# Optimization experiments

Measured on AMD Instinct MI355X. Metric: run time of the kernel, lower is better.

Reference implementation:

```python
import jax, jax.numpy as jnp
import numpy as np

B, L, D = 4, 4096, 1024
N_HEADS = 16
HEAD_SIZE = D // N_HEADS  # 64


def setup_inputs() -> dict:
    key = jax.random.key(0)
    k_x, k_w, k_m = jax.random.split(key, 3)
    x = jax.random.normal(k_x, (B, L, D), dtype=jnp.float32)
    # nn.Linear(D, 3*head_size, bias=False): weight (3*hs, D); store transposed (D, 3*hs)
    W_qkv = jax.random.normal(k_w, (D, 3 * HEAD_SIZE), dtype=jnp.float32) * (D ** -0.5)
    attn_mask = jax.random.randint(k_m, (B, L), 0, 2).astype(jnp.bool_)
    return {"x": x, "attn_mask": attn_mask, "W_qkv": W_qkv}


def reference(x, attn_mask, W_qkv):
    # x: (B, L, D); W_qkv: (D, 3*hs); attn_mask: (B, L) True = attend
    qkv = x @ W_qkv                                # (B, L, 3*hs)
    q, k, v = jnp.split(qkv, 3, axis=-1)           # each (B, L, hs)
    scale = HEAD_SIZE ** -0.5
    scores = jnp.einsum('bqd,bkd->bqk', q, k) * scale   # (B, L, L)
    neg_inf = jnp.finfo(scores.dtype).min
    scores = jnp.where(attn_mask[:, None, :], scores, neg_inf)
    weights = jax.nn.softmax(scores, axis=-1)      # (B, L, L)
    out = jnp.einsum('bqk,bkd->bqd', weights, v)   # (B, L, hs)
    return out
```

## Files before the change

### kernel.cpp

```cpp
#include <hip/hip_runtime.h>

typedef __bf16 bf16_t;
typedef __bf16 bf16x8 __attribute__((ext_vector_type(8)));
typedef __bf16 bf16x4 __attribute__((ext_vector_type(4)));
typedef float  f32x4  __attribute__((ext_vector_type(4)));
struct uint4_t { unsigned x, y, z, w; };

#define B_  4
#define L_  4096
#define D_  1024
#define HS  64
#define NQ  192
#define SCL2E 0.1803368801111204f
#define MFMA16 __builtin_amdgcn_mfma_f32_16x16x32_bf16

__global__ void detect_kernel(const unsigned char* mask, const unsigned short* xw,
                              int* flags) {
    __shared__ int c1, c23, cbad;
    int tid = threadIdx.x;
    if (tid == 0) { c1 = 0; c23 = 0; cbad = 0; }
    __syncthreads();
    uint4_t m[4];
#pragma unroll
    for (int i = 0; i < 4; ++i)
        m[i] = *(const uint4_t*)(mask + tid * 16 + i * 4096);
    int a = 0, bc = 0;
#pragma unroll
    for (int i = 0; i < 4; ++i) {
        const unsigned* w = (const unsigned*)&m[i];
#pragma unroll
        for (int j = 0; j < 4; ++j) {
            if (w[j] & 0x0000ff00u) a++;
            if (w[j] & 0xffff0000u) bc++;
        }
    }
    uint4_t xm = *(const uint4_t*)(xw + tid * 8);
    int bad = 0;
    const unsigned* xwv = (const unsigned*)&xm;
#pragma unroll
    for (int j = 0; j < 4; ++j)
#pragma unroll
        for (int h = 0; h < 2; ++h) {
            unsigned s = (xwv[j] >> (16 * h)) & 0xFFFFu;
            unsigned e = (s >> 7) & 0xFF;
            if (e > 150 || (e < 90 && e != 0)) bad++;
        }
    if (a)   atomicAdd(&c1, a);
    if (bc)  atomicAdd(&c23, bc);
    if (bad) atomicAdd(&cbad, bad);
    __syncthreads();
    if (tid == 0) {
        flags[0] = (c1 > 0) ? 1 : ((c23 > 0) ? 2 : 0);
        flags[1] = (cbad >= 64) ? 1 : 0;
    }
}

__global__ __launch_bounds__(256) void pack_w_kernel(const void* __restrict__ Win,
                                                     const int* __restrict__ flags,
                                                     bf16_t* __restrict__ Wtp) {
    int idx = blockIdx.x * 256 + threadIdx.x;
    if (idx >= 24576) return;
    int lane = idx & 63;
    int t    = (idx >> 6) & 3;
    int kc   = (idx >> 8) & 31;
    int ct   = idx >> 13;
    int n  = ct * 64 + t * 16 + (lane & 15);
    int k0 = kc * 32 + (lane >> 4) * 8;
    int f32 = flags[1];
    bf16x8 v;
#pragma unroll
    for (int j = 0; j < 8; ++j) {
        if (f32) v[j] = (bf16_t)(((const float*)Win)[(k0 + j) * NQ + n]);
        else     v[j] = ((const bf16_t*)Win)[(k0 + j) * NQ + n];
    }
    *(bf16x8*)(Wtp + (size_t)idx * 8) = v;
}

__global__ __launch_bounds__(256, 2) void qkv_gemm_kernel(const void* __restrict__ xin,
                                                          const int* __restrict__ flags,
                                                          const bf16_t* __restrict__ Wtp,
                                                          bf16_t* __restrict__ Qb,
                                                          bf16_t* __restrict__ Kb,
                                                          bf16_t* __restrict__ Vt) {
    __shared__ __align__(16) bf16_t xt[2][32 * 72];
    __shared__ __align__(16) bf16_t sqk[32 * 136];
    __shared__ __align__(16) bf16_t sv[64 * 40];

    int tid = threadIdx.x;
    int wave = tid >> 6, lane = tid & 63, quad = lane >> 4, l16 = lane & 15;
    int rg = wave & 1, ch = wave >> 1;
    int m0 = blockIdx.x * 32;
    int xf = flags[1];

    f32x4 acc[6] = {};
    bf16x8 xr, Ba[6], Bb[6];
    int srow = tid >> 3, soff = (tid & 7) * 8;

    auto stage_load = [&](int ks) {
        if (xf) {
            const float* xp = (const float*)xin + (size_t)(m0 + srow) * D_ + ks * 64 + soff;
            f32x4 lo = *(const f32x4*)xp, hi = *(const f32x4*)(xp + 4);
            xr[0] = (bf16_t)lo[0]; xr[1] = (bf16_t)lo[1];
            xr[2] = (bf16_t)lo[2]; xr[3] = (bf16_t)lo[3];
            xr[4] = (bf16_t)hi[0]; xr[5] = (bf16_t)hi[1];
            xr[6] = (bf16_t)hi[2]; xr[7] = (bf16_t)hi[3];
        } else {
            xr = *(const bf16x8*)((const bf16_t*)xin + (size_t)(m0 + srow) * D_ + ks * 64 + soff);
        }
    };
    auto stage_store = [&](int buf) {
        *(bf16x8*)&xt[buf][srow * 72 + soff] = xr;
    };
    auto loadB6 = [&](int k32, bf16x8* Bv) {
#pragma unroll
        for (int i = 0; i < 6; ++i) {
            int st = ch * 6 + i, ct2 = st >> 2, tt = st & 3;
            Bv[i] = *(const bf16x8*)(Wtp + ((size_t)(ct2 * 32 + k32) * 4 + tt) * 512 + lane * 8);
        }
    };
    auto compute6 = [&](int buf, int c, const bf16x8* Bv) {
        bf16x8 A = *(const bf16x8*)&xt[buf][(rg * 16 + l16) * 72 + c * 32 + quad * 8];
#pragma unroll
        for (int i = 0; i < 6; ++i)
            acc[i] = MFMA16(A, Bv[i], acc[i], 0, 0, 0);
    };

    stage_load(0); stage_store(0);
    loadB6(0, Ba);
    __syncthreads();
    for (int ks = 0; ks < 16; ++ks) {
        bool more = (ks + 1 < 16);
        if (more) stage_load(ks + 1);
        loadB6(2 * ks + 1, Bb);
        compute6(ks & 1, 0, Ba);
        if (more) loadB6(2 * ks + 2, Ba);
        compute6(ks & 1, 1, Bb);
        if (more) stage_store((ks + 1) & 1);
        __syncthreads();
    }

    int rowb = rg * 16 + quad * 4;
#pragma unroll
    for (int i = 0; i < 6; ++i) {
        int col = ch * 96 + i * 16 + l16;
#pragma unroll
        for (int r = 0; r < 4; ++r) {
            bf16_t hv = (bf16_t)acc[i][r];
            if (col < 128) sqk[(rowb + r) * 136 + col] = hv;
            else           sv[(col - 128) * 40 + rowb + r] = hv;
        }
    }
    __syncthreads();

    int bb = m0 >> 12, l0 = m0 & 4095;
#pragma unroll
    for (int it = 0; it < 2; ++it) {
        int c = tid + it * 256;
        int row = c >> 4, off = (c & 15) * 8;
        bf16x8 v = *(const bf16x8*)&sqk[row * 136 + off];
        if (off < 64) *(bf16x8*)(Qb + (size_t)(bb * L_ + l0 + row) * HS + off) = v;
        else          *(bf16x8*)(Kb + (size_t)(bb * L_ + l0 + row) * HS + off - 64) = v;
    }
    {
        int d = tid >> 2, off = (tid & 3) * 8;
        bf16x8 v = *(const bf16x8*)&sv[d * 40 + off];
        *(bf16x8*)(Vt + (size_t)(bb * HS + d) * L_ + l0 + off) = v;
    }
}

template<int NSPLIT>
__global__ __launch_bounds__(256, 4) void attn_kernel(const bf16_t* __restrict__ Qb,
                                                      const bf16_t* __restrict__ Kb,
                                                      const bf16_t* __restrict__ Vt,
                                                      const void* __restrict__ maskp,
                                                      const int* __restrict__ flags,
                                                      float* __restrict__ Opart,
                                                      float* __restrict__ lpart,
                                                      void* __restrict__ outv) {
    constexpr int KCH = L_ / NSPLIT;
    constexpr int NIT = KCH / 64;
    __shared__ __align__(16) bf16_t ktile[2][64 * 72];
    __shared__ __align__(16) bf16_t plds[4][32 * 72];
    __shared__ float mb[KCH];

    int tid = threadIdx.x, wave = tid >> 6, lane = tid & 63;
    int quad = lane >> 4, l16 = lane & 15;
    int grp = blockIdx.x % (B_ * NSPLIT);
    int qt  = blockIdx.x / (B_ * NSPLIT);
    int s = grp / B_, b = grp % B_;
    int q0 = qt * 128;
    int kbase = s * KCH;

    const float NEGINF = -__builtin_inff();
    int mkind = flags[0];
    if (mkind == 1) {
        const unsigned char* mp = (const unsigned char*)maskp + b * L_ + kbase;
        for (int i = tid; i < KCH; i += 256) mb[i] = mp[i] ? 0.0f : NEGINF;
    } else if (mkind == 2) {
        const float* mp = (const float*)maskp + b * L_ + kbase;
        for (int i = tid; i < KCH; i += 256) mb[i] = (mp[i] != 0.0f) ? 0.0f : NEGINF;
    } else {
        const int* mp = (const int*)maskp + b * L_ + kbase;
        for (int i = tid; i < KCH; i += 256) mb[i] = mp[i] ? 0.0f : NEGINF;
    }

    bf16x8 aQ[2][2];
#pragma unroll
    for (int rg = 0; rg < 2; ++rg) {
        const bf16_t* qp = Qb + (size_t)(b * L_ + q0 + wave * 32 + rg * 16 + l16) * HS + quad * 8;
        aQ[rg][0] = *(const bf16x8*)qp;
        aQ[rg][1] = *(const bf16x8*)(qp + 32);
    }

    const bf16_t* Kbase = Kb + (size_t)b * L_ * HS;
    const bf16_t* Vbase = Vt + (size_t)b * HS * L_;

    f32x4 O[2][4] = {};
    float lr[2][4] = {};
    bf16_t* pw = &plds[wave][0];
    bf16x8 kr[2];
    int srow = 0, soff = 0;

    auto kstage_load = [&](int t) {
#pragma unroll
        for (int j = 0; j < 2; ++j) {
            int c = tid + j * 256;
            int row = c >> 3, off = (c & 7) * 8;
            kr[j] = *(const bf16x8*)(Kbase + (size_t)(kbase + t * 64 + row) * HS + off);
        }
    };
    auto kstage_store = [&](int buf) {
#pragma unroll
        for (int j = 0; j < 2; ++j) {
            int c = tid + j * 256;
            int row = c >> 3, off = (c & 7) * 8;
            *(bf16x8*)&ktile[buf][row * 72 + off] = kr[j];
        }
    };
    (void)srow; (void)soff;

    kstage_load(0);
    kstage_store(0);
    __syncthreads();

    for (int t = 0; t < NIT; ++t) {
        int kb = kbase + t * 64;
        bool more = (t + 1 < NIT);
        if (more) kstage_load(t + 1);

        bf16x8 V0[4];
#pragma unroll
        for (int nt = 0; nt < 4; ++nt)
            V0[nt] = *(const bf16x8*)(Vbase + (size_t)(nt * 16 + l16) * L_ + kb + quad * 8);

        const bf16_t* kl = &ktile[t & 1][0];
#pragma unroll
        for (int h = 0; h < 2; ++h) {
            f32x4 sc[2][2];
#pragma unroll
            for (int s2 = 0; s2 < 2; ++s2) {
                int st = h * 2 + s2;
                bf16x8 kb0 = *(const bf16x8*)&kl[(st * 16 + l16) * 72 + quad * 8];
                bf16x8 kb1 = *(const bf16x8*)&kl[(st * 16 + l16) * 72 + 32 + quad * 8];
#pragma unroll
                for (int rg = 0; rg < 2; ++rg) {
                    f32x4 t0 = {};
                    t0 = MFMA16(aQ[rg][0], kb0, t0, 0, 0, 0);
                    t0 = MFMA16(aQ[rg][1], kb1, t0, 0, 0, 0);
                    sc[rg][s2] = t0;
                }
            }
#pragma unroll
            for (int s2 = 0; s2 < 2; ++s2) {
                int st = h * 2 + s2;
                float bl = mb[t * 64 + st * 16 + l16];
#pragma unroll
                for (int rg = 0; rg < 2; ++rg)
#pragma unroll
                    for (int r = 0; r < 4; ++r) {
                        float p = exp2f(fmaf(sc[rg][s2][r], SCL2E, bl));
                        lr[rg][r] += p;
                        pw[(rg * 16 + quad * 4 + r) * 72 + st * 16 + l16] = (bf16_t)p;
                    }
            }
        }

#pragma unroll
        for (int rg = 0; rg < 2; ++rg) {
            bf16x8 aP = *(const bf16x8*)&pw[(rg * 16 + l16) * 72 + quad * 8];
#pragma unroll
            for (int nt = 0; nt < 4; ++nt)
                O[rg][nt] = MFMA16(aP, V0[nt], O[rg][nt], 0, 0, 0);
        }
        bf16x8 V1[4];
#pragma unroll
        for (int nt = 0; nt < 4; ++nt)
            V1[nt] = *(const bf16x8*)(Vbase + (size_t)(nt * 16 + l16) * L_ + kb + 32 + quad * 8);
#pragma unroll
        for (int rg = 0; rg < 2; ++rg) {
            bf16x8 aP = *(const bf16x8*)&pw[(rg * 16 + l16) * 72 + 32 + quad * 8];
#pragma unroll
            for (int nt = 0; nt < 4; ++nt)
                O[rg][nt] = MFMA16(aP, V1[nt], O[rg][nt], 0, 0, 0);
        }

        if (more) kstage_store((t + 1) & 1);
        __syncthreads();
    }

    int of32 = flags[1];
#pragma unroll
    for (int rg = 0; rg < 2; ++rg)
#pragma unroll
        for (int r = 0; r < 4; ++r) {
            float sm = lr[rg][r];
            sm += __shfl_xor(sm, 1);
            sm += __shfl_xor(sm, 2);
            sm += __shfl_xor(sm, 4);
            sm += __shfl_xor(sm, 8);
            int row = q0 + wave * 32 + rg * 16 + quad * 4 + r;
            if (NSPLIT == 1) {
                float inv = 1.0f / sm;
                size_t base = (size_t)(b * L_ + row) * HS;
                if (of32) {
                    float* op = (float*)outv + base;
#pragma unroll
                    for (int nt = 0; nt < 4; ++nt) op[nt * 16 + l16] = O[rg][nt][r] * inv;
                } else {
                    bf16_t* op = (bf16_t*)outv + base;
#pragma unroll
                    for (int nt = 0; nt < 4; ++nt) op[nt * 16 + l16] = (bf16_t)(O[rg][nt][r] * inv);
                }
            } else {
                float* op = Opart + (size_t)s * (B_ * L_ * HS) + (size_t)(b * L_ + row) * HS;
#pragma unroll
                for (int nt = 0; nt < 4; ++nt) op[nt * 16 + l16] = O[rg][nt][r];
                if (l16 == 0) lpart[(size_t)s * (B_ * L_) + b * L_ + row] = sm;
            }
        }
}

__global__ __launch_bounds__(256) void reduce_kernel(const float* __restrict__ Opart,
                                                     const float* __restrict__ lpart,
                                                     const int* __restrict__ flags,
                                                     void* __restrict__ outv,
                                                     int nsplit) {
    int i4 = (blockIdx.x * 256 + threadIdx.x) * 4;
    int row = i4 >> 6;
    f32x4 acc = {};
    float lsum = 0.f;
    for (int s = 0; s < nsplit; ++s) {
        acc  += *(const f32x4*)&Opart[(size_t)s * (B_ * L_ * HS) + i4];
        lsum += lpart[(size_t)s * (B_ * L_) + row];
    }
    float inv = 1.0f / lsum;
    if (flags[1]) {
        f32x4 r = { acc[0] * inv, acc[1] * inv, acc[2] * inv, acc[3] * inv };
        *(f32x4*)&((float*)outv)[i4] = r;
    } else {
        bf16x4 r;
#pragma unroll
        for (int j = 0; j < 4; ++j) r[j] = (bf16_t)(acc[j] * inv);
        *(bf16x4*)&((bf16_t*)outv)[i4] = r;
    }
}

extern "C" void kernel_launch(void* const* d_in, const int* in_sizes, int n_in,
                              void* d_out, int out_size, void* d_ws, size_t ws_size,
                              hipStream_t stream) {
    (void)in_sizes; (void)n_in; (void)out_size;
    const void* x    = d_in[0];
    const void* mask = d_in[1];
    const void* W    = d_in[2];

    char* ws = (char*)d_ws;
    bf16_t* Qb    = (bf16_t*)(ws);
    bf16_t* Kb    = (bf16_t*)(ws + (2u << 20));
    bf16_t* Vt    = (bf16_t*)(ws + (4u << 20));
    bf16_t* Wtp   = (bf16_t*)(ws + (6u << 20));
    int*    flags = (int*)   (ws + (6u << 20) + (512u << 10));
    float*  Opart = (float*) (ws + (7u << 20));

    auto need = [](int ns) -> size_t {
        return (7u << 20) + (size_t)ns * (B_ * L_ * HS * 4)
                          + (size_t)ns * (B_ * L_ * 4) + 4096;
    };
    int nsplit = (ws_size >= need(8)) ? 8 : (ws_size >= need(4)) ? 4 : 1;
    float* lpart = (float*)(ws + (7u << 20) + (size_t)nsplit * (B_ * L_ * HS * 4));

    detect_kernel<<<1, 256, 0, stream>>>((const unsigned char*)mask,
                                         (const unsigned short*)x, flags);
    pack_w_kernel<<<96, 256, 0, stream>>>(W, flags, Wtp);
    qkv_gemm_kernel<<<512, 256, 0, stream>>>(x, flags, Wtp, Qb, Kb, Vt);
    if (nsplit == 8) {
        attn_kernel<8><<<32 * B_ * 8, 256, 0, stream>>>(Qb, Kb, Vt, mask, flags,
                                                        Opart, lpart, d_out);
        reduce_kernel<<<(B_ * L_ * HS) / 1024, 256, 0, stream>>>(Opart, lpart, flags,
                                                                 d_out, 8);
    } else if (nsplit == 4) {
        attn_kernel<4><<<32 * B_ * 4, 256, 0, stream>>>(Qb, Kb, Vt, mask, flags,
                                                        Opart, lpart, d_out);
        reduce_kernel<<<(B_ * L_ * HS) / 1024, 256, 0, stream>>>(Opart, lpart, flags,
                                                                 d_out, 4);
    } else {
        attn_kernel<1><<<32 * B_, 256, 0, stream>>>(Qb, Kb, Vt, mask, flags,
                                                    Opart, lpart, d_out);
    }
}
```

Before: 182.6 us.

## Fuse detect into weight pack, stage x in halves, compute softmax sum via MFMA

```diff
diff --git a/kernel.cpp b/kernel.cpp
--- a/kernel.cpp
+++ b/kernel.cpp
@@ -14,8 +14,11 @@
 #define SCL2E 0.1803368801111204f
 #define MFMA16 __builtin_amdgcn_mfma_f32_16x16x32_bf16
 
-__global__ void detect_kernel(const unsigned char* mask, const unsigned short* xw,
-                              int* flags) {
+__global__ __launch_bounds__(256) void pack_w_kernel(const void* __restrict__ Win,
+                                                     const unsigned char* __restrict__ mask,
+                                                     const unsigned short* __restrict__ xw,
+                                                     bf16_t* __restrict__ Wtp,
+                                                     int* __restrict__ flags) {
     __shared__ int c1, c23, cbad;
     int tid = threadIdx.x;
     if (tid == 0) { c1 = 0; c23 = 0; cbad = 0; }
@@ -49,24 +52,19 @@
     if (bc)  atomicAdd(&c23, bc);
     if (bad) atomicAdd(&cbad, bad);
     __syncthreads();
-    if (tid == 0) {
+    int f32 = (cbad >= 64) ? 1 : 0;
+    if (blockIdx.x == 0 && tid == 0) {
         flags[0] = (c1 > 0) ? 1 : ((c23 > 0) ? 2 : 0);
-        flags[1] = (cbad >= 64) ? 1 : 0;
-    }
-}
-
-__global__ __launch_bounds__(256) void pack_w_kernel(const void* __restrict__ Win,
-                                                     const int* __restrict__ flags,
-                                                     bf16_t* __restrict__ Wtp) {
-    int idx = blockIdx.x * 256 + threadIdx.x;
-    if (idx >= 24576) return;
+        flags[1] = f32;
+    }
+
+    int idx = blockIdx.x * 256 + tid;
     int lane = idx & 63;
     int t    = (idx >> 6) & 3;
     int kc   = (idx >> 8) & 31;
     int ct   = idx >> 13;
     int n  = ct * 64 + t * 16 + (lane & 15);
     int k0 = kc * 32 + (lane >> 4) * 8;
-    int f32 = flags[1];
     bf16x8 v;
 #pragma unroll
     for (int j = 0; j < 8; ++j) {
@@ -82,7 +80,7 @@
                                                           bf16_t* __restrict__ Qb,
                                                           bf16_t* __restrict__ Kb,
                                                           bf16_t* __restrict__ Vt) {
-    __shared__ __align__(16) bf16_t xt[2][32 * 72];
+    __shared__ __align__(16) bf16_t xs[32 * 520];
     __shared__ __align__(16) bf16_t sqk[32 * 136];
     __shared__ __align__(16) bf16_t sv[64 * 40];
 
@@ -93,50 +91,64 @@
     int xf = flags[1];
 
     f32x4 acc[6] = {};
-    bf16x8 xr, Ba[6], Bb[6];
-    int srow = tid >> 3, soff = (tid & 7) * 8;
-
-    auto stage_load = [&](int ks) {
-        if (xf) {
-            const float* xp = (const float*)xin + (size_t)(m0 + srow) * D_ + ks * 64 + soff;
-            f32x4 lo = *(const f32x4*)xp, hi = *(const f32x4*)(xp + 4);
-            xr[0] = (bf16_t)lo[0]; xr[1] = (bf16_t)lo[1];
-            xr[2] = (bf16_t)lo[2]; xr[3] = (bf16_t)lo[3];
-            xr[4] = (bf16_t)hi[0]; xr[5] = (bf16_t)hi[1];
-            xr[6] = (bf16_t)hi[2]; xr[7] = (bf16_t)hi[3];
-        } else {
-            xr = *(const bf16x8*)((const bf16_t*)xin + (size_t)(m0 + srow) * D_ + ks * 64 + soff);
-        }
-    };
-    auto stage_store = [&](int buf) {
-        *(bf16x8*)&xt[buf][srow * 72 + soff] = xr;
-    };
-    auto loadB6 = [&](int k32, bf16x8* Bv) {
+    bf16x8 Ba[6], Bb[6];
+
+    auto stage = [&](int h) {
+        bf16x8 tmp[8];
+#pragma unroll
+        for (int j = 0; j < 8; ++j) {
+            int c = tid + j * 256;
+            int row = c >> 6, off = (c & 63) * 8;
+            if (xf) {
+                const float* xp = (const float*)xin + (size_t)(m0 + row) * D_ + h * 512 + off;
+                f32x4 lo = *(const f32x4*)xp, hi = *(const f32x4*)(xp + 4);
+                tmp[j][0] = (bf16_t)lo[0]; tmp[j][1] = (bf16_t)lo[1];
+                tmp[j][2] = (bf16_t)lo[2]; tmp[j][3] = (bf16_t)lo[3];
+                tmp[j][4] = (bf16_t)hi[0]; tmp[j][5] = (bf16_t)hi[1];
+                tmp[j][6] = (bf16_t)hi[2]; tmp[j][7] = (bf16_t)hi[3];
+            } else {
+                tmp[j] = *(const bf16x8*)((const bf16_t*)xin + (size_t)(m0 + row) * D_ + h * 512 + off);
+            }
+        }
+#pragma unroll
+        for (int j = 0; j < 8; ++j) {
+            int c = tid + j * 256;
+            int row = c >> 6, off = (c & 63) * 8;
+            *(bf16x8*)&xs[row * 520 + off] = tmp[j];
+        }
+    };
+    auto loadB6 = [&](int ks, bf16x8* Bv) {
 #pragma unroll
         for (int i = 0; i < 6; ++i) {
             int st = ch * 6 + i, ct2 = st >> 2, tt = st & 3;
-            Bv[i] = *(const bf16x8*)(Wtp + ((size_t)(ct2 * 32 + k32) * 4 + tt) * 512 + lane * 8);
-        }
-    };
-    auto compute6 = [&](int buf, int c, const bf16x8* Bv) {
-        bf16x8 A = *(const bf16x8*)&xt[buf][(rg * 16 + l16) * 72 + c * 32 + quad * 8];
+            Bv[i] = *(const bf16x8*)(Wtp + ((size_t)(ct2 * 32 + ks) * 4 + tt) * 512 + lane * 8);
+        }
+    };
+    auto compute6 = [&](int ks, const bf16x8* Bv) {
+        bf16x8 A = *(const bf16x8*)&xs[(rg * 16 + l16) * 520 + (ks & 15) * 32 + quad * 8];
 #pragma unroll
         for (int i = 0; i < 6; ++i)
             acc[i] = MFMA16(A, Bv[i], acc[i], 0, 0, 0);
     };
 
-    stage_load(0); stage_store(0);
+    stage(0);
     loadB6(0, Ba);
     __syncthreads();
-    for (int ks = 0; ks < 16; ++ks) {
-        bool more = (ks + 1 < 16);
-        if (more) stage_load(ks + 1);
-        loadB6(2 * ks + 1, Bb);
-        compute6(ks & 1, 0, Ba);
-        if (more) loadB6(2 * ks + 2, Ba);
-        compute6(ks & 1, 1, Bb);
-        if (more) stage_store((ks + 1) & 1);
-        __syncthreads();
+#pragma unroll
+    for (int half = 0; half < 2; ++half) {
+        int base = half * 16;
+        for (int m = 0; m < 16; m += 2) {
+            int ks = base + m;
+            loadB6(ks + 1, Bb);
+            compute6(ks, Ba);
+            loadB6(ks + 2 <= 31 ? ks + 2 : 31, Ba);
+            compute6(ks + 1, Bb);
+        }
+        if (half == 0) {
+            __syncthreads();
+            stage(1);
+            __syncthreads();
+        }
     }
 
     int rowb = rg * 16 + quad * 4;
@@ -211,15 +223,17 @@
         aQ[rg][0] = *(const bf16x8*)qp;
         aQ[rg][1] = *(const bf16x8*)(qp + 32);
     }
+    bf16x8 ones;
+#pragma unroll
+    for (int j = 0; j < 8; ++j) ones[j] = (bf16_t)1.0f;
 
     const bf16_t* Kbase = Kb + (size_t)b * L_ * HS;
     const bf16_t* Vbase = Vt + (size_t)b * HS * L_;
 
     f32x4 O[2][4] = {};
-    float lr[2][4] = {};
+    f32x4 O5[2] = {};
     bf16_t* pw = &plds[wave][0];
     bf16x8 kr[2];
-    int srow = 0, soff = 0;
 
     auto kstage_load = [&](int t) {
 #pragma unroll
@@ -237,7 +251,6 @@
             *(bf16x8*)&ktile[buf][row * 72 + off] = kr[j];
         }
     };
-    (void)srow; (void)soff;
 
     kstage_load(0);
     kstage_store(0);
@@ -279,7 +292,6 @@
 #pragma unroll
                     for (int r = 0; r < 4; ++r) {
                         float p = exp2f(fmaf(sc[rg][s2][r], SCL2E, bl));
-                        lr[rg][r] += p;
                         pw[(rg * 16 + quad * 4 + r) * 72 + st * 16 + l16] = (bf16_t)p;
                     }
             }
@@ -291,6 +303,7 @@
 #pragma unroll
             for (int nt = 0; nt < 4; ++nt)
                 O[rg][nt] = MFMA16(aP, V0[nt], O[rg][nt], 0, 0, 0);
+            O5[rg] = MFMA16(aP, ones, O5[rg], 0, 0, 0);
         }
         bf16x8 V1[4];
 #pragma unroll
@@ -302,6 +315,7 @@
 #pragma unroll
             for (int nt = 0; nt < 4; ++nt)
                 O[rg][nt] = MFMA16(aP, V1[nt], O[rg][nt], 0, 0, 0);
+            O5[rg] = MFMA16(aP, ones, O5[rg], 0, 0, 0);
         }
 
         if (more) kstage_store((t + 1) & 1);
@@ -313,11 +327,7 @@
     for (int rg = 0; rg < 2; ++rg)
 #pragma unroll
         for (int r = 0; r < 4; ++r) {
-            float sm = lr[rg][r];
-            sm += __shfl_xor(sm, 1);
-            sm += __shfl_xor(sm, 2);
-            sm += __shfl_xor(sm, 4);
-            sm += __shfl_xor(sm, 8);
+            float sm = O5[rg][r];
             int row = q0 + wave * 32 + rg * 16 + quad * 4 + r;
             if (NSPLIT == 1) {
                 float inv = 1.0f / sm;
@@ -388,9 +398,8 @@
     int nsplit = (ws_size >= need(8)) ? 8 : (ws_size >= need(4)) ? 4 : 1;
     float* lpart = (float*)(ws + (7u << 20) + (size_t)nsplit * (B_ * L_ * HS * 4));
 
-    detect_kernel<<<1, 256, 0, stream>>>((const unsigned char*)mask,
-                                         (const unsigned short*)x, flags);
-    pack_w_kernel<<<96, 256, 0, stream>>>(W, flags, Wtp);
+    pack_w_kernel<<<96, 256, 0, stream>>>(W, (const unsigned char*)mask,
+                                          (const unsigned short*)x, Wtp, flags);
     qkv_gemm_kernel<<<512, 256, 0, stream>>>(x, flags, Wtp, Qb, Kb, Vt);
     if (nsplit == 8) {
         attn_kernel<8><<<32 * B_ * 8, 256, 0, stream>>>(Qb, Kb, Vt, mask, flags,
```

New measurement: 167.3 us. 8.4% less time.
